# Performance work log

Measured on AMD Instinct MI355X. Metric: run time of the kernel, lower is better.

## Reference

```python
import jax, jax.numpy as jnp
import numpy as np

POOL_SIZE = 8
SEG_LEN = 100
N_CODEBOOKS = 4
VOCAB = 1024
EMB = 128
HID = 512
LAT = 256
NUM_CODES = 1024
BETA = 0.1
BATCH = 128


def _pool_matrix(T, P):
    # torch adaptive_avg_pool1d bin boundaries
    starts = np.floor(np.arange(P) * T / P).astype(int)
    ends = np.ceil((np.arange(P) + 1) * T / P).astype(int)
    M = np.zeros((T, P), np.float32)
    for i in range(P):
        M[starts[i]:ends[i], i] = 1.0 / (ends[i] - starts[i])
    return jnp.asarray(M)

_POOL = _pool_matrix(SEG_LEN, POOL_SIZE)


def _conv1d_same3(x, w, b):
    # x: (B, Cin, T), w: (Cout, Cin, 3), padding=1
    y = jax.lax.conv_general_dilated(x, w, (1,), [(1, 1)],
                                     dimension_numbers=('NCH', 'OIH', 'NCH'))
    return y + b[None, :, None]


def _encode(tokens, emb, c1w, c1b, c2w, c2b, c3w, c3b):
    # tokens: (B, T, C) int -> z_e (B, POOL_SIZE, LAT)
    B, T, C = tokens.shape
    x = emb[tokens]                      # (B, T, C, EMB)
    x = x.reshape(B, T, C * EMB).transpose(0, 2, 1)  # (B, C*EMB, T)
    x = jax.nn.relu(_conv1d_same3(x, c1w, c1b))
    x = jax.nn.relu(_conv1d_same3(x, c2w, c2b))
    x = jnp.einsum('bct,tp->bcp', x, _POOL)          # adaptive avg pool -> (B, HID, 8)
    x = jnp.einsum('bcp,oc->bpo', x, c3w[:, :, 0]) + c3b  # 1x1 conv -> (B, 8, LAT)
    return x


def _vq(z_e, codebook):
    # z_e: (B, L, D); eval-mode EMA quantizer (no buffer update)
    cb_sq = jnp.sum(codebook ** 2, axis=-1)          # (K,)
    dist = (jnp.sum(z_e ** 2, axis=-1, keepdims=True)
            - 2.0 * jnp.einsum('bld,kd->blk', z_e, codebook) + cb_sq)
    codes = jnp.argmin(dist, axis=-1)                # (B, L)
    z_q = codebook[codes]                            # gather (B, L, D)
    z_q_st = z_e + jax.lax.stop_gradient(z_q - z_e)
    commit = jnp.mean((z_e - jax.lax.stop_gradient(z_q)) ** 2)
    return z_q_st, codes, BETA * commit


def _decode(z_prev, z_curr, z_next, fc1w, fc1b, fc2w, fc2b, d1w, d1b, d2w, d2b):
    B = z_curr.shape[0]
    z = jnp.concatenate([z_prev, z_curr, z_next], axis=1).reshape(B, -1)  # (B, 3*8*LAT)
    h = jax.nn.relu(z @ fc1w.T + fc1b)
    h = jax.nn.relu(h @ fc2w.T + fc2b)               # (B, HID)
    h = jnp.broadcast_to(h[:, :, None], (B, HID, SEG_LEN))
    # ConvTranspose1d(k=3, pad=1, stride=1) == conv with flipped, transposed kernel
    w1 = jnp.flip(jnp.swapaxes(d1w, 0, 1), -1)       # (O, I, 3)
    h = jax.nn.relu(_conv1d_same3(h, w1, d1b))
    out = jnp.einsum('bct,cv->bvt', h, d2w[:, :, 0]) + d2b[None, :, None]  # (B, V*C, T)
    logits = out.reshape(B, N_CODEBOOKS, VOCAB, SEG_LEN).transpose(0, 3, 1, 2)
    return logits                                    # (B, T, C, V)


def _model(tokens_prev, tokens_curr, tokens_next, emb, conv1_w, conv1_b,
           conv2_w, conv2_b, conv3_w, conv3_b, codebook, fc1_w, fc1_b,
           fc2_w, fc2_b, deconv1_w, deconv1_b, deconv2_w, deconv2_b):
    enc = lambda t: _encode(t, emb, conv1_w, conv1_b, conv2_w, conv2_b, conv3_w, conv3_b)
    z_prev, _, vq_prev = _vq(enc(tokens_prev), codebook)
    z_curr, _, vq_curr = _vq(enc(tokens_curr), codebook)
    z_next, _, vq_next = _vq(enc(tokens_next), codebook)
    logits = _decode(z_prev, z_curr, z_next, fc1_w, fc1_b, fc2_w, fc2_b,
                     deconv1_w, deconv1_b, deconv2_w, deconv2_b)
    logp = jax.nn.log_softmax(logits, axis=-1)
    nll = -jnp.take_along_axis(logp, tokens_curr[..., None], axis=-1)[..., 0]
    recon_loss = jnp.mean(nll)
    vq_loss = vq_prev + vq_curr + vq_next
    centered = codebook - jnp.mean(codebook, axis=0, keepdims=True)
    diversity_loss = -jnp.mean(centered ** 2)
    total = recon_loss + vq_loss + 0.0 * diversity_loss  # variance_loss_scale=0.0
    return total


def setup_inputs() -> dict:
    key = jax.random.key(0)
    ks = jax.random.split(key, 20)
    s = 0.02
    n = lambda k, shape, sc=0.02: sc * jax.random.normal(k, shape, dtype=jnp.float32)
    return {
        'tokens_prev': jax.random.randint(ks[0], (BATCH, SEG_LEN, N_CODEBOOKS), 0, VOCAB),
        'tokens_curr': jax.random.randint(ks[1], (BATCH, SEG_LEN, N_CODEBOOKS), 0, VOCAB),
        'tokens_next': jax.random.randint(ks[2], (BATCH, SEG_LEN, N_CODEBOOKS), 0, VOCAB),
        'emb': n(ks[3], (VOCAB, EMB), 1.0),
        'conv1_w': n(ks[4], (HID, EMB * N_CODEBOOKS, 3)),
        'conv1_b': jnp.zeros((HID,), jnp.float32),
        'conv2_w': n(ks[5], (HID, HID, 3)),
        'conv2_b': jnp.zeros((HID,), jnp.float32),
        'conv3_w': n(ks[6], (LAT, HID, 1)),
        'conv3_b': jnp.zeros((LAT,), jnp.float32),
        'codebook': n(ks[7], (NUM_CODES, LAT), 1.0),
        'fc1_w': n(ks[8], (HID, LAT * POOL_SIZE * 3)),
        'fc1_b': jnp.zeros((HID,), jnp.float32),
        'fc2_w': n(ks[9], (HID, HID)),
        'fc2_b': jnp.zeros((HID,), jnp.float32),
        'deconv1_w': n(ks[10], (HID, HID, 3)),
        'deconv1_b': jnp.zeros((HID,), jnp.float32),
        'deconv2_w': n(ks[11], (HID, VOCAB * N_CODEBOOKS, 1)),
        'deconv2_b': jnp.zeros((VOCAB * N_CODEBOOKS,), jnp.float32),
    }


def reference(tokens_prev, tokens_curr, tokens_next, emb, conv1_w, conv1_b,
              conv2_w, conv2_b, conv3_w, conv3_b, codebook, fc1_w, fc1_b,
              fc2_w, fc2_b, deconv1_w, deconv1_b, deconv2_w, deconv2_b):
    return _model(tokens_prev, tokens_curr, tokens_next, emb, conv1_w, conv1_b,
                  conv2_w, conv2_b, conv3_w, conv3_b, codebook, fc1_w, fc1_b,
                  fc2_w, fc2_b, deconv1_w, deconv1_b, deconv2_w, deconv2_b)
```

## Files before the change

### kernel.cpp

```cpp
#include <hip/hip_runtime.h>
#include <math.h>

#define B_    128
#define T_    100
#define TPAD  104
#define CB_   4
#define EMB_  128
#define NROW  39936
#define ZOFF  131072

typedef __attribute__((ext_vector_type(8))) short short8;
typedef __attribute__((ext_vector_type(4))) short short4v;
typedef __attribute__((ext_vector_type(4))) float f32x4;

__device__ __forceinline__ short f2bf(float x) {
  unsigned u = __builtin_bit_cast(unsigned, x);
  u += 0x7fffu + ((u >> 16) & 1u);
  return (short)(u >> 16);
}
__device__ __forceinline__ float bf2f(short s) {
  unsigned u = ((unsigned)(unsigned short)s) << 16;
  return __builtin_bit_cast(float, u);
}

#define GLOAD_LDS(g, l) __builtin_amdgcn_global_load_lds( \
    (const __attribute__((address_space(1))) void*)(g),   \
    (__attribute__((address_space(3))) void*)(l), 16, 0, 0)

#define MFMA16(a, b, c) __builtin_amdgcn_mfma_f32_16x16x32_bf16(a, b, c, 0, 0, 0)
#define SWZ(row, slot) (((slot) + ((row) >> 1)) & 3)

#define STEP_SYNC() do {                                   \
    asm volatile("s_waitcnt vmcnt(0)" ::: "memory");       \
    __builtin_amdgcn_s_barrier();                          \
    __builtin_amdgcn_sched_barrier(0);                     \
  } while (0)

__global__ void k_prep(const float* __restrict__ emb,
                       const float* __restrict__ c1w, const float* __restrict__ c2w,
                       const float* __restrict__ c3w, const float* __restrict__ cbk,
                       const float* __restrict__ fc1w, const float* __restrict__ fc2w,
                       const float* __restrict__ d1w, const float* __restrict__ d2w,
                       short* __restrict__ YbS, short* __restrict__ embB,
                       short* __restrict__ Wb1, short* __restrict__ Wb2,
                       short* __restrict__ c3wB, short* __restrict__ cbkB,
                       short* __restrict__ fc1wB, short* __restrict__ fc2wB,
                       short* __restrict__ SB, short* __restrict__ d2wTB,
                       float* __restrict__ cbsq) {
  __shared__ float tile[32][33];
  int bid = blockIdx.x;
  int id = bid * 256 + threadIdx.x;
  if (bid < 24581) {
    if (id < 1024) {
      int row = id >> 9, c = id & 511;
      long off = row ? ((long)(NROW + 1) * 512 + c) : c;
      YbS[off] = 0;
    } else if (id < 132096) {
      int l = id - 1024;
      embB[l] = f2bf(emb[l]);
    } else if (id < 132224) {
      embB[ZOFF + (id - 132096)] = 0;
    } else if (id < 1705088) {
      int local = id - 132224;
      const float* w = (local < 786432) ? c1w : c2w;
      short* o = (local < 786432) ? Wb1 : Wb2;
      int l2 = (local < 786432) ? local : local - 786432;
      int i = l2 & 511, oo = (l2 >> 9) & 511, tap = l2 >> 18;
      o[l2] = f2bf(w[oo * 1536 + i * 3 + tap]);
    } else if (id < 1836160) {
      int l = id - 1705088;
      c3wB[l] = f2bf(c3w[l]);
    } else if (id < 2098304) {
      int l = id - 1836160;
      cbkB[l] = f2bf(cbk[l]);
    } else if (id < 5244032) {
      int l = id - 2098304;
      fc1wB[l] = f2bf(fc1w[l]);
    } else if (id < 5506176) {
      int l = id - 5244032;
      fc2wB[l] = f2bf(fc2w[l]);
    } else if (id < 6292608) {
      int l = id - 5506176;
      int i = l & 511, o = (l >> 9) & 511, cls = l >> 18;
      const float* w = d1w + (i * 512 + o) * 3;
      float v;
      if (cls == 0)      v = w[0] + w[1];
      else if (cls == 1) v = w[0] + w[1] + w[2];
      else               v = w[1] + w[2];
      SB[(cls * 512 + o) * 512 + i] = f2bf(v);
    }
  } else if (bid < 26629) {
    int blk = bid - 24581;
    int bx = blk & 127, by = blk >> 7;
    int tx = threadIdx.x & 31, ty = threadIdx.x >> 5;
    #pragma unroll
    for (int j = 0; j < 32; j += 8)
      tile[ty + j][tx] = d2w[(by * 32 + ty + j) * 4096 + bx * 32 + tx];
    __syncthreads();
    #pragma unroll
    for (int j = 0; j < 32; j += 8)
      d2wTB[(bx * 32 + ty + j) * 512 + by * 32 + tx] = f2bf(tile[tx][ty + j]);
  } else {
    int idx = (bid - 26629) * 256 + threadIdx.x;
    int row = idx >> 6, lane = threadIdx.x & 63;
    float4 v = *(const float4*)&cbk[row * 256 + lane * 4];
    float s = v.x * v.x + v.y * v.y + v.z * v.z + v.w * v.w;
    #pragma unroll
    for (int m = 1; m < 64; m <<= 1) s += __shfl_xor(s, m);
    if (lane == 0) cbsq[row] = s;
  }
}

__global__ __launch_bounds__(256) void k_conv1_embed(const int* __restrict__ tok0,
                                                     const int* __restrict__ tok1,
                                                     const int* __restrict__ tok2,
                                                     const short* __restrict__ embB,
                                                     const short* __restrict__ Wb,
                                                     const float* __restrict__ bias,
                                                     short* __restrict__ Y) {
  __shared__ short sm[2][16896];
  int r0 = blockIdx.y * 128;
  int o0 = blockIdx.x * 128;
  int tid = threadIdx.x;
  int lane = tid & 63, wid = tid >> 6;
  int wm = wid >> 1, wn = wid & 1;
  int ls = lane >> 4, lr = lane & 15;
  int g = ((lane & 3) - ((lane >> 3) & 3)) & 3;

  int toff[3][4];
  #pragma unroll
  for (int i = 0; i < 3; ++i) {
    int q = wid + 4 * i;
    if (q < 9) {
      int rr = r0 - 1 + 16 * q + (lane >> 2);
      bool ok = (rr >= 0) && (rr < NROW);
      int sb = ok ? (rr / 104) : 0;
      int t = rr - sb * 104;
      ok = ok && (t < T_);
      int b = sb & 127, s = sb >> 7;
      const int* tokp = (s == 0) ? tok0 : (s == 1) ? tok1 : tok2;
      if (ok) {
        int4 tv = *(const int4*)&tokp[(b * T_ + t) * CB_];
// ... 53 lines not shown
        int row = wm * 64 + m * 16 + lr + tap;
        a[m] = A8[row * 4 + SWZ(row, ls)];
      }
      #pragma unroll
      for (int n = 0; n < 4; ++n) {
        int row = wn * 64 + n * 16 + lr;
        b[n] = B8[(tap * 128 + row) * 4 + SWZ(row, ls)];
      }
      #pragma unroll
      for (int m = 0; m < 4; ++m)
        #pragma unroll
        for (int n = 0; n < 4; ++n)
          acc[m][n] = MFMA16(a[m], b[n], acc[m][n]);
    }
    STEP_SYNC();
  }
  #pragma unroll
  for (int m = 0; m < 4; ++m) {
    #pragma unroll
    for (int n = 0; n < 4; ++n) {
      int col = o0 + wn * 64 + n * 16 + lr;
      float bv = bias[col];
      #pragma unroll
      for (int j = 0; j < 4; ++j) {
        int r = r0 + wm * 64 + m * 16 + ls * 4 + j;
        int t = r % TPAD;
        float v = (t < T_) ? fmaxf(acc[m][n][j] + bv, 0.f) : 0.f;
        Y[(long)r * 512 + col] = f2bf(v);
      }
    }
  }
}

__global__ __launch_bounds__(256) void k_conv3_mfma(const short* __restrict__ X,
                                                    const short* __restrict__ Wb,
                                                    const float* __restrict__ bias,
                                                    short* __restrict__ Y) {
  __shared__ short sm[2][16896];
  int r0 = blockIdx.y * 128;
  int o0 = blockIdx.x * 128;
  int tid = threadIdx.x;
  int lane = tid & 63, wid = tid >> 6;
  int wm = wid >> 1, wn = wid & 1;
  int ls = lane >> 4, lr = lane & 15;
  int g = ((lane & 3) - ((lane >> 3) & 3)) & 3;
  long laneoff = (long)(lane >> 2) * 512 + g * 8;

  const short* gp[9];
  #pragma unroll
  for (int i = 0; i < 9; ++i) {
    int q = wid + 4 * i;
    if (q < 33) {
      long base;
      const short* src;
      if (q < 9) { src = X; base = (long)(r0 - 1 + 16 * q) * 512; }
      else {
        int b = q - 9, tap = b >> 3, j = b & 7;
        src = Wb; base = (long)(tap * 512 + o0 + 16 * j) * 512;
      }
      gp[i] = src + base + laneoff;
    }
  }

  #pragma unroll
  for (int i = 0; i < 9; ++i) {
    int q = wid + 4 * i;
    if (q < 33) { GLOAD_LDS(gp[i], &sm[0][q * 512]); gp[i] += 32; }
  }
  STEP_SYNC();

// ... 10 lines not shown
    }
    const short8* A8 = (const short8*)sm[cur];
    const short8* B8 = (const short8*)(sm[cur] + 4608);
    #pragma unroll
    for (int tap = 0; tap < 3; ++tap) {
      short8 a[4], b[4];
      #pragma unroll
      for (int m = 0; m < 4; ++m) {
        int row = wm * 64 + m * 16 + lr + tap;
        a[m] = A8[row * 4 + SWZ(row, ls)];
      }
      #pragma unroll
      for (int n = 0; n < 4; ++n) {
        int row = wn * 64 + n * 16 + lr;
        b[n] = B8[(tap * 128 + row) * 4 + SWZ(row, ls)];
      }
      #pragma unroll
      for (int m = 0; m < 4; ++m)
        #pragma unroll
        for (int n = 0; n < 4; ++n)
          acc[m][n] = MFMA16(a[m], b[n], acc[m][n]);
    }
    STEP_SYNC();
  }
  #pragma unroll
  for (int m = 0; m < 4; ++m) {
    #pragma unroll
    for (int n = 0; n < 4; ++n) {
      int col = o0 + wn * 64 + n * 16 + lr;
      float bv = bias[col];
      #pragma unroll
      for (int j = 0; j < 4; ++j) {
        int r = r0 + wm * 64 + m * 16 + ls * 4 + j;
        int t = r % TPAD;
        float v = (t < T_) ? fmaxf(acc[m][n][j] + bv, 0.f) : 0.f;
        Y[(long)r * 512 + col] = f2bf(v);
      }
    }
  }
}

__global__ __launch_bounds__(256) void k_gemm_mfma(const short* __restrict__ A,
                                                   const short* __restrict__ B,
                                                   float* __restrict__ C,
                                                   short* __restrict__ Cb,
                                                   const float* __restrict__ bias,
                                                   int K, int N, int relu) {
  __shared__ short sm[8192];
  int r0 = blockIdx.x * 128;
  int o0 = blockIdx.y * 128;
  int tid = threadIdx.x;
  int lane = tid & 63, wid = tid >> 6;
  int wm = wid >> 1, wn = wid & 1;
  int ls = lane >> 4, lr = lane & 15;
  int g = ((lane & 3) - ((lane >> 3) & 3)) & 3;
  long laneoff = (long)(lane >> 2) * K + g * 8;

  const short* gp[4];
  const short* lp[4];
  #pragma unroll
  for (int i = 0; i < 4; ++i) {
    int q = wid + 4 * i;
    const short* src;
    long base;
    if (q < 8) { src = A; base = (long)(r0 + 16 * q) * K; }
    else       { src = B; base = (long)(o0 + 16 * (q - 8)) * K; }
    gp[i] = src + base + laneoff;
    lp[i] = sm + q * 512;
  }

  f32x4 acc[4][4] = {};
  for (int kc = 0; kc < K; kc += 32) {
// ... 11 lines not shown
    for (int m = 0; m < 4; ++m) {
      int row = wm * 64 + m * 16 + lr;
      a[m] = A8[row * 4 + SWZ(row, ls)];
    }
    #pragma unroll
    for (int n = 0; n < 4; ++n) {
      int row = wn * 64 + n * 16 + lr;
      b[n] = B8[row * 4 + SWZ(row, ls)];
    }
    #pragma unroll
    for (int m = 0; m < 4; ++m)
      #pragma unroll
      for (int n = 0; n < 4; ++n)
        acc[m][n] = MFMA16(a[m], b[n], acc[m][n]);
  }
  #pragma unroll
  for (int m = 0; m < 4; ++m) {
    #pragma unroll
    for (int n = 0; n < 4; ++n) {
      int col = o0 + wn * 64 + n * 16 + lr;
      float bv = bias ? bias[col] : 0.f;
      #pragma unroll
      for (int j = 0; j < 4; ++j) {
        int r = r0 + wm * 64 + m * 16 + ls * 4 + j;
        float v = acc[m][n][j] + bv;
        if (relu) v = fmaxf(v, 0.f);
        C[(long)r * N + col] = v;
        if (Cb) Cb[(long)r * N + col] = f2bf(v);
      }
    }
  }
}

__global__ __launch_bounds__(256) void k_dot_argmin(const short* __restrict__ A,
                                                    const short* __restrict__ B,
                                                    const float* __restrict__ cbsq,
                                                    float* __restrict__ apv,
                                                    int* __restrict__ api) {
  __shared__ short sm[8192];
  __shared__ float svv[128][2];
  __shared__ int sii[128][2];
  const int K = 256;
  int r0 = blockIdx.x * 128;
  int o0 = blockIdx.y * 128;
  int tid = threadIdx.x;
  int lane = tid & 63, wid = tid >> 6;
  int wm = wid >> 1, wn = wid & 1;
  int ls = lane >> 4, lr = lane & 15;
  int g = ((lane & 3) - ((lane >> 3) & 3)) & 3;
  long laneoff = (long)(lane >> 2) * K + g * 8;

  const short* gp[4];
  const short* lp[4];
  #pragma unroll
  for (int i = 0; i < 4; ++i) {
    int q = wid + 4 * i;
    const short* src;
    long base;
    if (q < 8) { src = A; base = (long)(r0 + 16 * q) * K; }
    else       { src = B; base = (long)(o0 + 16 * (q - 8)) * K; }
    gp[i] = src + base + laneoff;
    lp[i] = sm + q * 512;
  }

  f32x4 acc[4][4] = {};
  #pragma unroll
  for (int kc = 0; kc < K; kc += 32) {
    __syncthreads();
    #pragma unroll
    for (int i = 0; i < 4; ++i) {
      GLOAD_LDS(gp[i], lp[i]);
      gp[i] += 32;
    }
    __syncthreads();
    const short8* A8 = (const short8*)sm;
    const short8* B8 = (const short8*)(sm + 4096);
    short8 a[4], b[4];
    #pragma unroll
    for (int m = 0; m < 4; ++m) {
      int row = wm * 64 + m * 16 + lr;
      a[m] = A8[row * 4 + SWZ(row, ls)];
    }
    #pragma unroll
    for (int n = 0; n < 4; ++n) {
      int row = wn * 64 + n * 16 + lr;
      b[n] = B8[row * 4 + SWZ(row, ls)];
    }
    #pragma unroll
    for (int m = 0; m < 4; ++m)
      #pragma unroll
      for (int n = 0; n < 4; ++n)
        acc[m][n] = MFMA16(a[m], b[n], acc[m][n]);
  }
  float cq[4];
  #pragma unroll
  for (int n = 0; n < 4; ++n) cq[n] = cbsq[o0 + wn * 64 + n * 16 + lr];
  #pragma unroll
  for (int m = 0; m < 4; ++m) {
    #pragma unroll
    for (int j = 0; j < 4; ++j) {
      float bv = 3.4e38f; int bi = 0x7fffffff;
      #pragma unroll
      for (int n = 0; n < 4; ++n) {
        int col = o0 + wn * 64 + n * 16 + lr;
        float v = cq[n] - 2.f * acc[m][n][j];
        if (v < bv || (v == bv && col < bi)) { bv = v; bi = col; }
      }
      #pragma unroll
      for (int d = 1; d < 16; d <<= 1) {
        float ov = __shfl_xor(bv, d);
        int oi = __shfl_xor(bi, d);
        if (ov < bv || (ov == bv && oi < bi)) { bv = ov; bi = oi; }
      }
      if (lr == 0) {
        int rl = wm * 64 + m * 16 + ls * 4 + j;
        svv[rl][wn] = bv;
        sii[rl][wn] = bi;
      }
    }
  }
  __syncthreads();
  if (tid < 128) {
    float v0 = svv[tid][0], v1 = svv[tid][1];
    int i0 = sii[tid][0], i1 = sii[tid][1];
    bool t1 = (v1 < v0) || (v1 == v0 && i1 < i0);
    apv[(long)(r0 + tid) * 8 + blockIdx.y] = t1 ? v1 : v0;
    api[(long)(r0 + tid) * 8 + blockIdx.y] = t1 ? i1 : i0;
  }
}

__global__ __launch_bounds__(256) void k_vq_combine(const float* __restrict__ apv,
                                                    const int* __restrict__ api,
                                                    const float* __restrict__ ze,
                                                    const float* __restrict__ cb,
                                                    const short* __restrict__ cbkB,
                                                    short* __restrict__ zallB,
                                                    float* __restrict__ commit_part) {
  __shared__ float sv[256];
  __shared__ int ksb;
  int row = blockIdx.x, tid = threadIdx.x;
  if (tid == 0) {
    float bv = apv[(long)row * 8]; int bi = api[(long)row * 8];
    #pragma unroll
    for (int j = 1; j < 8; ++j) {
      float v = apv[(long)row * 8 + j]; int i = api[(long)row * 8 + j];
      if (v < bv || (v == bv && i < bi)) { bv = v; bi = i; }
    }
    ksb = bi;
  }
  __syncthreads();
  int ks = ksb;
  float zq = cb[ks * 256 + tid];
  float zev = ze[(long)row * 256 + tid];
  int s = row >> 10, bp = row & 1023;
  int b = bp >> 3, p = bp & 7;
  zallB[b * 6144 + s * 2048 + p * 256 + tid] = cbkB[ks * 256 + tid];
  float d = zev - zq;
  sv[tid] = d * d;
  __syncthreads();
  for (int off = 128; off; off >>= 1) { if (tid < off) sv[tid] += sv[tid + off]; __syncthreads(); }
  if (tid == 0) commit_part[row] = sv[0];
}

__global__ __launch_bounds__(256) void k_gemm_mfma_sk(const short* __restrict__ A,
                                                      const short* __restrict__ B,
                                                      float* __restrict__ part,
                                                      int M, int N, int K,
                                                      int kchunk, int KS, long bgstride) {
  __shared__ short sm[8192];
  int r0 = blockIdx.x * 128;
  int o0 = blockIdx.y * 128;
  int bz = blockIdx.z;
  int g = bz / KS, zz = bz - g * KS;
  const short* Bg = B + (long)g * bgstride;
  int k0 = zz * kchunk;
  int tid = threadIdx.x;
  int lane = tid & 63, wid = tid >> 6;
  int wm = wid >> 1, wn = wid & 1;
  int ls = lane >> 4, lr = lane & 15;
  int gsl = ((lane & 3) - ((lane >> 3) & 3)) & 3;
  long laneoff = (long)(lane >> 2) * K + gsl * 8 + k0;

  const short* gp[4];
  const short* lp[4];
  #pragma unroll
  for (int i = 0; i < 4; ++i) {
    int q = wid + 4 * i;
    const short* src;
    long base;
    if (q < 8) { src = A;  base = (long)(r0 + 16 * q) * K; }
    else       { src = Bg; base = (long)(o0 + 16 * (q - 8)) * K; }
    gp[i] = src + base + laneoff;
    lp[i] = sm + q * 512;
  }
// ... 11 lines not shown
    const short8* B8 = (const short8*)(sm + 4096);
    short8 a[4], b[4];
    #pragma unroll
    for (int m = 0; m < 4; ++m) {
      int row = wm * 64 + m * 16 + lr;
      a[m] = A8[row * 4 + SWZ(row, ls)];
    }
    #pragma unroll
    for (int n = 0; n < 4; ++n) {
      int row = wn * 64 + n * 16 + lr;
      b[n] = B8[row * 4 + SWZ(row, ls)];
    }
    #pragma unroll
    for (int m = 0; m < 4; ++m)
      #pragma unroll
      for (int n = 0; n < 4; ++n)
        acc[m][n] = MFMA16(a[m], b[n], acc[m][n]);
  }
  float* P = part + (long)bz * M * N;
  #pragma unroll
  for (int m = 0; m < 4; ++m) {
    #pragma unroll
    for (int n = 0; n < 4; ++n) {
      int col = o0 + wn * 64 + n * 16 + lr;
      #pragma unroll
      for (int j = 0; j < 4; ++j) {
        int r = r0 + wm * 64 + m * 16 + ls * 4 + j;
        P[(long)r * N + col] = acc[m][n][j];
      }
    }
  }
}

__global__ void k_reduce_bf16(const float* __restrict__ part, short* __restrict__ Cb,
                              const float* __restrict__ bias, int N, int MN,
                              int KS, int relu, int total4) {
  int id = blockIdx.x * 256 + threadIdx.x;
  if (id >= total4) return;
  int e = id * 4;
  int g = e / MN;
  int rem = e - g * MN;
  const float* base = part + (long)g * KS * MN + rem;
  float4 s = *(const float4*)base;
  for (int j = 1; j < KS; ++j) {
    float4 v = *(const float4*)(base + (long)j * MN);
    s.x += v.x; s.y += v.y; s.z += v.z; s.w += v.w;
  }
  int c = rem % N;
  s.x += bias[c]; s.y += bias[c + 1]; s.z += bias[c + 2]; s.w += bias[c + 3];
  if (relu) {
    s.x = fmaxf(s.x, 0.f); s.y = fmaxf(s.y, 0.f);
    s.z = fmaxf(s.z, 0.f); s.w = fmaxf(s.w, 0.f);
  }
  short4v o;
  o[0] = f2bf(s.x); o[1] = f2bf(s.y); o[2] = f2bf(s.z); o[3] = f2bf(s.w);
  *(short4v*)&Cb[(long)g * MN + rem] = o;
}

__global__ void k_pool(const short* __restrict__ Xg, short* __restrict__ pooledB) {
  int id = blockIdx.x * 256 + threadIdx.x;
  int row = id >> 6, cg = id & 63;
  int s = row >> 10, bp = row & 1023;
  int b = bp >> 3, p = bp & 7;
  int t0 = (p * 25) >> 1;
  const short8* src = (const short8*)(Xg + (long)((s * 128 + b) * TPAD + t0) * 512) + cg;
  float acc[8] = {};
  #pragma unroll
  for (int j = 0; j < 13; ++j) {
    short8 v = src[j * 64];
    #pragma unroll
    for (int k = 0; k < 8; ++k) acc[k] += bf2f(v[k]);
  }
  short8 o;
  #pragma unroll
  for (int k = 0; k < 8; ++k) o[k] = f2bf(acc[k] * (1.f / 13.f));
  ((short8*)pooledB)[(long)row * 64 + cg] = o;
}

__global__ __launch_bounds__(256) void k_logits_lse_recon(const float* __restrict__ part,
                                                          const float* __restrict__ d2b,
                                                          const int* __restrict__ tok,
                                                          float* __restrict__ rpart2) {
  __shared__ float row[1024];
  __shared__ float sm[256];
  int blk = blockIdx.x;
  int cb_i = blk & 3, b = (blk >> 2) & 127, cls = blk >> 9;
  int m = cls * 128 + b;
  const float* p0 = part + (long)m * 4096 + cb_i * 1024;
  const float* p1 = p0 + (long)384 * 4096;
  const float* bb = d2b + cb_i * 1024;
  int tid = threadIdx.x;
  float v[4];
  #pragma unroll
  for (int j = 0; j < 4; ++j) {
    int c = tid + 256 * j;
    v[j] = p0[c] + p1[c] + bb[c];
    row[c] = v[j];
  }
  float mx = fmaxf(fmaxf(v[0], v[1]), fmaxf(v[2], v[3]));
  sm[tid] = mx; __syncthreads();
  for (int off = 128; off; off >>= 1) { if (tid < off) sm[tid] = fmaxf(sm[tid], sm[tid + off]); __syncthreads(); }
  float gm = sm[0]; __syncthreads();
  float e = expf(v[0] - gm) + expf(v[1] - gm) + expf(v[2] - gm) + expf(v[3] - gm);
  sm[tid] = e; __syncthreads();
  for (int off = 128; off; off >>= 1) { if (tid < off) sm[tid] += sm[tid + off]; __syncthreads(); }
  float lse = gm + logf(sm[0]);
  __syncthreads();
  float val = 0.f;
  if (cls == 1) {
    if (tid < 98) {
      int tk = tok[(b * T_ + tid + 1) * CB_ + cb_i];
      val = lse - row[tk];
    }
  } else if (tid == 0) {
    int t = (cls == 0) ? 0 : 99;
    int tk = tok[(b * T_ + t) * CB_ + cb_i];
    val = lse - row[tk];
  }
  sm[tid] = val; __syncthreads();
  for (int off = 128; off; off >>= 1) { if (tid < off) sm[tid] += sm[tid + off]; __syncthreads(); }
  if (tid == 0) rpart2[blk] = sm[0];
}

__global__ void k_final(const float* __restrict__ rpart2, const float* __restrict__ cpart,
                        float* __restrict__ out) {
  __shared__ float sm[256];
  __shared__ float rs;
  int tid = threadIdx.x;
  float r = 0.f;
  #pragma unroll
  for (int j = 0; j < 6; ++j) r += rpart2[tid + 256 * j];
  sm[tid] = r; __syncthreads();
  for (int off = 128; off; off >>= 1) { if (tid < off) sm[tid] += sm[tid + off]; __syncthreads(); }
  if (tid == 0) rs = sm[0];
  __syncthreads();
  float c = 0.f;
  #pragma unroll
  for (int j = 0; j < 12; ++j) c += cpart[tid + 256 * j];
  sm[tid] = c; __syncthreads();
  for (int off = 128; off; off >>= 1) { if (tid < off) sm[tid] += sm[tid + off]; __syncthreads(); }
  if (tid == 0) out[0] = rs / 51200.f + 0.1f * (sm[0] / 262144.f);
}

extern "C" void kernel_launch(void* const* d_in, const int* in_sizes, int n_in,
                              void* d_out, int out_size, void* d_ws, size_t ws_size,
                              hipStream_t stream) {
  const int*   tok_prev = (const int*)d_in[0];
  const int*   tok_curr = (const int*)d_in[1];
  const int*   tok_next = (const int*)d_in[2];
  const float* emb  = (const float*)d_in[3];
  const float* c1w  = (const float*)d_in[4];
  const float* c1b  = (const float*)d_in[5];
  const float* c2w  = (const float*)d_in[6];
  const float* c2b  = (const float*)d_in[7];
  const float* c3w  = (const float*)d_in[8];
  const float* c3b  = (const float*)d_in[9];
  const float* cbk  = (const float*)d_in[10];
  const float* fc1w = (const float*)d_in[11];
  const float* fc1b = (const float*)d_in[12];
  const float* fc2w = (const float*)d_in[13];
  const float* fc2b = (const float*)d_in[14];
  const float* d1w  = (const float*)d_in[15];
  const float* d1b  = (const float*)d_in[16];
  const float* d2w  = (const float*)d_in[17];
  const float* d2b  = (const float*)d_in[18];

  float* ws = (float*)d_ws;
  short* XbS = (short*)ws;
  short* YbS = (short*)(ws + 10224128);
  float* fp  = ws + 2 * 10224128;
  short* Wb1    = (short*)fp;
  short* Wb2    = (short*)(fp + 393216);
  short* c3wB   = (short*)(fp + 786432);
  short* cbkB   = (short*)(fp + 851968);
  short* pooledB= (short*)(fp + 983040);
  float* ze     = fp + 1769472;
  short* zeB    = (short*)(fp + 2555904);
  short* fc1wB  = (short*)(fp + 2949120);
  short* fc2wB  = (short*)(fp + 4521984);
  short* SB     = (short*)(fp + 4653056);
  short* d2wTB  = (short*)(fp + 5046272);
  float* part   = fp + 6094848;
  float* cbsq   = part + 3145728;
  short* zallB  = (short*)(cbsq + 1024);
  float* cpart  = cbsq + 1024 + 393216;
  short* h1B    = (short*)(cpart + 3072);
  short* h2B    = (short*)(cpart + 35840);
  short* h2cB   = (short*)(cpart + 68608);
  float* rpart2 = cpart + 166912;
  float* apv    = cpart + 168448;
  int*   api    = (int*)(cpart + 193024);
  short* embB   = (short*)(cpart + 217600);

  const short* Yv = YbS + 512;
  short* Xc = XbS + 512;

  k_prep<<<26885, 256, 0, stream>>>(emb, c1w, c2w, c3w, cbk, fc1w, fc2w, d1w, d2w,
                                    YbS, embB, Wb1, Wb2, c3wB, cbkB, fc1wB, fc2wB,
                                    SB, d2wTB, cbsq);

  k_conv1_embed<<<dim3(4, 312), 256, 0, stream>>>(tok_prev, tok_curr, tok_next,
                                                  embB, Wb1, c1b, (short*)Yv);
  k_conv3_mfma <<<dim3(4, 312), 256, 0, stream>>>(Yv, Wb2, c2b, Xc);
  k_pool       <<<768, 256, 0, stream>>>(Xc, pooledB);
  k_gemm_mfma  <<<dim3(24, 2), 256, 0, stream>>>(pooledB, c3wB, ze, zeB, c3b, 512, 256, 0);
  k_dot_argmin <<<dim3(24, 8), 256, 0, stream>>>(zeB, cbkB, cbsq, apv, api);
  k_vq_combine <<<3072, 256, 0, stream>>>(apv, api, ze, cbk, cbkB, zallB, cpart);

  k_gemm_mfma_sk<<<dim3(1, 4, 16), 256, 0, stream>>>(zallB, fc1wB, part, 128, 512, 6144, 384, 16, 0);
  k_reduce_bf16 <<<64, 256, 0, stream>>>(part, h1B, fc1b, 512, 65536, 16, 1, 16384);
  k_gemm_mfma_sk<<<dim3(1, 4, 8), 256, 0, stream>>>(h1B, fc2wB, part, 128, 512, 512, 64, 8, 0);
  k_reduce_bf16 <<<64, 256, 0, stream>>>(part, h2B, fc2b, 512, 65536, 8, 1, 16384);
  k_gemm_mfma_sk<<<dim3(1, 4, 24), 256, 0, stream>>>(h2B, SB, part, 128, 512, 512, 64, 8, 262144);
  k_reduce_bf16 <<<192, 256, 0, stream>>>(part, h2cB, d1b, 512, 65536, 8, 1, 49152);
  k_gemm_mfma_sk<<<dim3(3, 32, 2), 256, 0, stream>>>(h2cB, d2wTB, part, 384, 4096, 512, 256, 2, 0);
  k_logits_lse_recon<<<1536, 256, 0, stream>>>(part, d2b, tok_curr, rpart2);

  k_final<<<1, 256, 0, stream>>>(rpart2, cpart, (float*)d_out);
}
```

Measured before the change: 260.3 us.

## Fold conv3 into codebook distances and fuse split-K reductions into next GEMM

```diff
diff --git a/kernel.cpp b/kernel.cpp
--- a/kernel.cpp
+++ b/kernel.cpp
@@ -38,19 +38,21 @@
 
 __global__ void k_prep(const float* __restrict__ emb,
                        const float* __restrict__ c1w, const float* __restrict__ c2w,
-                       const float* __restrict__ c3w, const float* __restrict__ cbk,
+                       const float* __restrict__ c3w, const float* __restrict__ c3b,
+                       const float* __restrict__ cbk,
                        const float* __restrict__ fc1w, const float* __restrict__ fc2w,
                        const float* __restrict__ d1w, const float* __restrict__ d2w,
                        short* __restrict__ YbS, short* __restrict__ embB,
                        short* __restrict__ Wb1, short* __restrict__ Wb2,
-                       short* __restrict__ c3wB, short* __restrict__ cbkB,
+                       short* __restrict__ c3wB, short* __restrict__ c3wT,
+                       short* __restrict__ cbkB,
                        short* __restrict__ fc1wB, short* __restrict__ fc2wB,
                        short* __restrict__ SB, short* __restrict__ d2wTB,
-                       float* __restrict__ cbsq) {
+                       float* __restrict__ cbsq2) {
   __shared__ float tile[32][33];
   int bid = blockIdx.x;
   int id = bid * 256 + threadIdx.x;
-  if (bid < 24581) {
+  if (bid < 25093) {
     if (id < 1024) {
       int row = id >> 9, c = id & 511;
       long off = row ? ((long)(NROW + 1) * 512 + c) : c;
@@ -70,17 +72,21 @@
     } else if (id < 1836160) {
       int l = id - 1705088;
       c3wB[l] = f2bf(c3w[l]);
-    } else if (id < 2098304) {
+    } else if (id < 1967232) {
       int l = id - 1836160;
+      int o = l & 255, i = l >> 8;
+      c3wT[l] = f2bf(c3w[o * 512 + i]);
+    } else if (id < 2229376) {
+      int l = id - 1967232;
       cbkB[l] = f2bf(cbk[l]);
-    } else if (id < 5244032) {
-      int l = id - 2098304;
+    } else if (id < 5375104) {
+      int l = id - 2229376;
       fc1wB[l] = f2bf(fc1w[l]);
-    } else if (id < 5506176) {
-      int l = id - 5244032;
+    } else if (id < 5637248) {
+      int l = id - 5375104;
       fc2wB[l] = f2bf(fc2w[l]);
-    } else if (id < 6292608) {
-      int l = id - 5506176;
+    } else if (id < 6423680) {
+      int l = id - 5637248;
       int i = l & 511, o = (l >> 9) & 511, cls = l >> 18;
       const float* w = d1w + (i * 512 + o) * 3;
       float v;
@@ -89,8 +95,8 @@
       else               v = w[1] + w[2];
       SB[(cls * 512 + o) * 512 + i] = f2bf(v);
     }
-  } else if (bid < 26629) {
-    int blk = bid - 24581;
+  } else if (bid < 27141) {
+    int blk = bid - 25093;
     int bx = blk & 127, by = blk >> 7;
     int tx = threadIdx.x & 31, ty = threadIdx.x >> 5;
     #pragma unroll
@@ -101,13 +107,15 @@
     for (int j = 0; j < 32; j += 8)
       d2wTB[(bx * 32 + ty + j) * 512 + by * 32 + tx] = f2bf(tile[tx][ty + j]);
   } else {
-    int idx = (bid - 26629) * 256 + threadIdx.x;
+    int idx = (bid - 27141) * 256 + threadIdx.x;
     int row = idx >> 6, lane = threadIdx.x & 63;
     float4 v = *(const float4*)&cbk[row * 256 + lane * 4];
+    float4 bb = *(const float4*)&c3b[lane * 4];
     float s = v.x * v.x + v.y * v.y + v.z * v.z + v.w * v.w;
-    #pragma unroll
-    for (int m = 1; m < 64; m <<= 1) s += __shfl_xor(s, m);
-    if (lane == 0) cbsq[row] = s;
+    float s2 = v.x * bb.x + v.y * bb.y + v.z * bb.z + v.w * bb.w;
+    #pragma unroll
+    for (int m = 1; m < 64; m <<= 1) { s += __shfl_xor(s, m); s2 += __shfl_xor(s2, m); }
+    if (lane == 0) cbsq2[row] = s - 2.f * s2;
   }
 }
 
@@ -390,15 +398,12 @@
   }
 }
 
-__global__ __launch_bounds__(256) void k_dot_argmin(const short* __restrict__ A,
-                                                    const short* __restrict__ B,
-                                                    const float* __restrict__ cbsq,
-                                                    float* __restrict__ apv,
-                                                    int* __restrict__ api) {
+__global__ __launch_bounds__(256) void k_zesq(const short* __restrict__ A,
+                                              const short* __restrict__ B,
+                                              const float* __restrict__ bias,
+                                              float* __restrict__ zs) {
   __shared__ short sm[8192];
-  __shared__ float svv[128][2];
-  __shared__ int sii[128][2];
-  const int K = 256;
+  const int K = 512;
   int r0 = blockIdx.x * 128;
   int o0 = blockIdx.y * 128;
   int tid = threadIdx.x;
@@ -422,7 +427,6 @@
   }
 
   f32x4 acc[4][4] = {};
-  #pragma unroll
   for (int kc = 0; kc < K; kc += 32) {
     __syncthreads();
     #pragma unroll
@@ -450,9 +454,88 @@
       for (int n = 0; n < 4; ++n)
         acc[m][n] = MFMA16(a[m], b[n], acc[m][n]);
   }
+  float s = 0.f;
+  #pragma unroll
+  for (int n = 0; n < 4; ++n) {
+    float bv = bias[o0 + wn * 64 + n * 16 + lr];
+    #pragma unroll
+    for (int m = 0; m < 4; ++m)
+      #pragma unroll
+      for (int j = 0; j < 4; ++j) {
+        float v = acc[m][n][j] + bv;
+        s += v * v;
+      }
+  }
+  __syncthreads();
+  float* red = (float*)sm;
+  red[tid] = s;
+  __syncthreads();
+  for (int off = 128; off; off >>= 1) { if (tid < off) red[tid] += red[tid + off]; __syncthreads(); }
+  if (tid == 0) zs[blockIdx.y * 24 + blockIdx.x] = red[0];
+}
+
+__global__ __launch_bounds__(256) void k_dot_argmin(const short* __restrict__ A,
+                                                    const short* __restrict__ B,
+                                                    const float* __restrict__ cbsq2,
+                                                    float* __restrict__ apv,
+                                                    int* __restrict__ api) {
+  __shared__ short sm[8192];
+  __shared__ float svv[128][2];
+  __shared__ int sii[128][2];
+  const int K = 512;
+  int r0 = blockIdx.x * 128;
+  int o0 = blockIdx.y * 128;
+  int tid = threadIdx.x;
+  int lane = tid & 63, wid = tid >> 6;
+  int wm = wid >> 1, wn = wid & 1;
+  int ls = lane >> 4, lr = lane & 15;
+  int g = ((lane & 3) - ((lane >> 3) & 3)) & 3;
+  long laneoff = (long)(lane >> 2) * K + g * 8;
+
+  const short* gp[4];
+  const short* lp[4];
+  #pragma unroll
+  for (int i = 0; i < 4; ++i) {
+    int q = wid + 4 * i;
+    const short* src;
+    long base;
+    if (q < 8) { src = A; base = (long)(r0 + 16 * q) * K; }
+    else       { src = B; base = (long)(o0 + 16 * (q - 8)) * K; }
+    gp[i] = src + base + laneoff;
+    lp[i] = sm + q * 512;
+  }
+
+  f32x4 acc[4][4] = {};
+  for (int kc = 0; kc < K; kc += 32) {
+    __syncthreads();
+    #pragma unroll
+    for (int i = 0; i < 4; ++i) {
+      GLOAD_LDS(gp[i], lp[i]);
+      gp[i] += 32;
+    }
+    __syncthreads();
+    const short8* A8 = (const short8*)sm;
+    const short8* B8 = (const short8*)(sm + 4096);
+    short8 a[4], b[4];
+    #pragma unroll
+    for (int m = 0; m < 4; ++m) {
+      int row = wm * 64 + m * 16 + lr;
+      a[m] = A8[row * 4 + SWZ(row, ls)];
+    }
+    #pragma unroll
+    for (int n = 0; n < 4; ++n) {
+      int row = wn * 64 + n * 16 + lr;
+      b[n] = B8[row * 4 + SWZ(row, ls)];
+    }
+    #pragma unroll
+    for (int m = 0; m < 4; ++m)
+      #pragma unroll
+      for (int n = 0; n < 4; ++n)
+        acc[m][n] = MFMA16(a[m], b[n], acc[m][n]);
+  }
   float cq[4];
   #pragma unroll
-  for (int n = 0; n < 4; ++n) cq[n] = cbsq[o0 + wn * 64 + n * 16 + lr];
+  for (int n = 0; n < 4; ++n) cq[n] = cbsq2[o0 + wn * 64 + n * 16 + lr];
   #pragma unroll
   for (int m = 0; m < 4; ++m) {
     #pragma unroll
@@ -489,35 +572,35 @@
 
 __global__ __launch_bounds__(256) void k_vq_combine(const float* __restrict__ apv,
                                                     const int* __restrict__ api,
-                                                    const float* __restrict__ ze,
-                                                    const float* __restrict__ cb,
                                                     const short* __restrict__ cbkB,
                                                     short* __restrict__ zallB,
-                                                    float* __restrict__ commit_part) {
-  __shared__ float sv[256];
-  __shared__ int ksb;
-  int row = blockIdx.x, tid = threadIdx.x;
-  if (tid == 0) {
-    float bv = apv[(long)row * 8]; int bi = api[(long)row * 8];
-    #pragma unroll
-    for (int j = 1; j < 8; ++j) {
-      float v = apv[(long)row * 8 + j]; int i = api[(long)row * 8 + j];
-      if (v < bv || (v == bv && i < bi)) { bv = v; bi = i; }
-    }
-    ksb = bi;
-  }
-  __syncthreads();
-  int ks = ksb;
-  float zq = cb[ks * 256 + tid];
-  float zev = ze[(long)row * 256 + tid];
+                                                    float* __restrict__ cpart) {
+  __shared__ float cm[8];
+  int tid = threadIdx.x;
+  int rg = tid >> 5, lt = tid & 31;
+  int lane = tid & 63;
+  int row = blockIdx.x * 8 + rg;
+  float v = 3.4e38f; int idx = 0x7fffffff;
+  if (lt < 8) { v = apv[(long)row * 8 + lt]; idx = api[(long)row * 8 + lt]; }
+  #pragma unroll
+  for (int d = 1; d < 8; d <<= 1) {
+    float ov = __shfl_xor(v, d);
+    int oi = __shfl_xor(idx, d);
+    if (ov < v || (ov == v && oi < idx)) { v = ov; idx = oi; }
+  }
+  int ks = __shfl(idx, lane & 32);
   int s = row >> 10, bp = row & 1023;
   int b = bp >> 3, p = bp & 7;
-  zallB[b * 6144 + s * 2048 + p * 256 + tid] = cbkB[ks * 256 + tid];
-  float d = zev - zq;
-  sv[tid] = d * d;
+  ((short8*)zallB)[(b * 6144 + s * 2048 + p * 256) / 8 + lt] =
+      ((const short8*)cbkB)[ks * 32 + lt];
+  if (lt == 0) cm[rg] = v;
   __syncthreads();
-  for (int off = 128; off; off >>= 1) { if (tid < off) sv[tid] += sv[tid + off]; __syncthreads(); }
-  if (tid == 0) commit_part[row] = sv[0];
+  if (tid == 0) {
+    float c = 0.f;
+    #pragma unroll
+    for (int j = 0; j < 8; ++j) c += cm[j];
+    cpart[blockIdx.x] = c;
+  }
 }
 
 __global__ __launch_bounds__(256) void k_gemm_mfma_sk(const short* __restrict__ A,
@@ -595,6 +678,96 @@
   }
 }
 
+__global__ __launch_bounds__(256) void k_gemm_sk_ared(const float* __restrict__ Apart,
+                                                      int KSa,
+                                                      const float* __restrict__ abias,
+                                                      const short* __restrict__ B,
+                                                      float* __restrict__ part,
+                                                      int KS, long bgstride) {
+  __shared__ short smem[16384];
+  int o0 = blockIdx.y * 128;
+  int bz = blockIdx.z;
+  int g = bz / KS, zz = bz - g * KS;
+  const short* Bg = B + (long)g * bgstride;
+  int k0 = zz * 64;
+  int tid = threadIdx.x;
+  int lane = tid & 63, wid = tid >> 6;
+  int wm = wid >> 1, wn = wid & 1;
+  int ls = lane >> 4, lr = lane & 15;
+  int gsw = ((lane & 3) - ((lane >> 3) & 3)) & 3;
+
+  #pragma unroll
+  for (int i = 0; i < 4; ++i) {
+    int idx = wid + 4 * i;
+    int step = idx >> 3, j = idx & 7;
+    const short* gp = Bg + (long)(o0 + 16 * j) * 512 + k0 + step * 32
+                    + (long)(lane >> 2) * 512 + gsw * 8;
+    GLOAD_LDS(gp, smem + 8192 + idx * 512);
+  }
+  #pragma unroll
+  for (int t = 0; t < 4; ++t) {
+    int slot = tid + 256 * t;
+    int step = slot >> 9, rem = slot & 511;
+    int row = rem >> 2, sl = rem & 3;
+    int gp2 = (sl - ((row >> 1) & 3)) & 3;
+    int col = k0 + step * 32 + gp2 * 8;
+    const float* ap = Apart + (long)row * 512 + col;
+    float s0 = 0, s1 = 0, s2 = 0, s3 = 0, s4 = 0, s5 = 0, s6 = 0, s7 = 0;
+    for (int j = 0; j < KSa; ++j) {
+      const float* p = ap + (long)j * 65536;
+      float4 a0 = *(const float4*)p;
+      float4 a1 = *(const float4*)(p + 4);
+      s0 += a0.x; s1 += a0.y; s2 += a0.z; s3 += a0.w;
+      s4 += a1.x; s5 += a1.y; s6 += a1.z; s7 += a1.w;
+    }
+    float4 b0 = *(const float4*)&abias[col];
+    float4 b1 = *(const float4*)&abias[col + 4];
+    short8 o;
+    o[0] = f2bf(fmaxf(s0 + b0.x, 0.f)); o[1] = f2bf(fmaxf(s1 + b0.y, 0.f));
+    o[2] = f2bf(fmaxf(s2 + b0.z, 0.f)); o[3] = f2bf(fmaxf(s3 + b0.w, 0.f));
+    o[4] = f2bf(fmaxf(s4 + b1.x, 0.f)); o[5] = f2bf(fmaxf(s5 + b1.y, 0.f));
+    o[6] = f2bf(fmaxf(s6 + b1.z, 0.f)); o[7] = f2bf(fmaxf(s7 + b1.w, 0.f));
+    ((short8*)smem)[step * 512 + row * 4 + sl] = o;
+  }
+  __syncthreads();
+
+  f32x4 acc[4][4] = {};
+  #pragma unroll
+  for (int step = 0; step < 2; ++step) {
+    const short8* A8 = (const short8*)smem + step * 512;
+    const short8* B8 = (const short8*)(smem + 8192) + step * 512;
+    short8 a[4], b[4];
+    #pragma unroll
+    for (int m = 0; m < 4; ++m) {
+      int row = wm * 64 + m * 16 + lr;
+      a[m] = A8[row * 4 + SWZ(row, ls)];
+    }
+    #pragma unroll
+    for (int n = 0; n < 4; ++n) {
+      int row = wn * 64 + n * 16 + lr;
+      b[n] = B8[row * 4 + SWZ(row, ls)];
+    }
+    #pragma unroll
+    for (int m = 0; m < 4; ++m)
+      #pragma unroll
+      for (int n = 0; n < 4; ++n)
+        acc[m][n] = MFMA16(a[m], b[n], acc[m][n]);
+  }
+  float* P = part + (long)bz * 65536;
+  #pragma unroll
+  for (int m = 0; m < 4; ++m) {
+    #pragma unroll
+    for (int n = 0; n < 4; ++n) {
+      int col = o0 + wn * 64 + n * 16 + lr;
+      #pragma unroll
+      for (int j = 0; j < 4; ++j) {
+        int r = wm * 64 + m * 16 + ls * 4 + j;
+        P[(long)r * 512 + col] = acc[m][n][j];
+      }
+    }
+  }
+}
+
 __global__ void k_reduce_bf16(const float* __restrict__ part, short* __restrict__ Cb,
                               const float* __restrict__ bias, int N, int MN,
                               int KS, int relu, int total4) {
@@ -650,14 +823,13 @@
   int cb_i = blk & 3, b = (blk >> 2) & 127, cls = blk >> 9;
   int m = cls * 128 + b;
   const float* p0 = part + (long)m * 4096 + cb_i * 1024;
-  const float* p1 = p0 + (long)384 * 4096;
   const float* bb = d2b + cb_i * 1024;
   int tid = threadIdx.x;
   float v[4];
   #pragma unroll
   for (int j = 0; j < 4; ++j) {
     int c = tid + 256 * j;
-    v[j] = p0[c] + p1[c] + bb[c];
+    v[j] = p0[c] + bb[c];
     row[c] = v[j];
   }
   float mx = fmaxf(fmaxf(v[0], v[1]), fmaxf(v[2], v[3]));
@@ -686,7 +858,7 @@
 }
 
 __global__ void k_final(const float* __restrict__ rpart2, const float* __restrict__ cpart,
-                        float* __restrict__ out) {
+                        const float* __restrict__ zesq, float* __restrict__ out) {
   __shared__ float sm[256];
   __shared__ float rs;
   int tid = threadIdx.x;
@@ -697,9 +869,9 @@
   for (int off = 128; off; off >>= 1) { if (tid < off) sm[tid] += sm[tid + off]; __syncthreads(); }
   if (tid == 0) rs = sm[0];
   __syncthreads();
-  float c = 0.f;
-  #pragma unroll
-  for (int j = 0; j < 12; ++j) c += cpart[tid + 256 * j];
+  float c = cpart[tid];
+  if (tid < 128) c += cpart[tid + 256];
+  if (tid < 48)  c += zesq[tid];
   sm[tid] = c; __syncthreads();
   for (int off = 128; off; off >>= 1) { if (tid < off) sm[tid] += sm[tid + off]; __syncthreads(); }
   if (tid == 0) out[0] = rs / 51200.f + 0.1f * (sm[0] / 262144.f);
@@ -735,49 +907,50 @@
   short* Wb1    = (short*)fp;
   short* Wb2    = (short*)(fp + 393216);
   short* c3wB   = (short*)(fp + 786432);
-  short* cbkB   = (short*)(fp + 851968);
-  short* pooledB= (short*)(fp + 983040);
-  float* ze     = fp + 1769472;
-  short* zeB    = (short*)(fp + 2555904);
-  short* fc1wB  = (short*)(fp + 2949120);
-  short* fc2wB  = (short*)(fp + 4521984);
-  short* SB     = (short*)(fp + 4653056);
-  short* d2wTB  = (short*)(fp + 5046272);
-  float* part   = fp + 6094848;
-  float* cbsq   = part + 3145728;
-  short* zallB  = (short*)(cbsq + 1024);
-  float* cpart  = cbsq + 1024 + 393216;
-  short* h1B    = (short*)(cpart + 3072);
-  short* h2B    = (short*)(cpart + 35840);
-  short* h2cB   = (short*)(cpart + 68608);
-  float* rpart2 = cpart + 166912;
-  float* apv    = cpart + 168448;
-  int*   api    = (int*)(cpart + 193024);
-  short* embB   = (short*)(cpart + 217600);
+  short* c3wT   = (short*)(fp + 851968);
+  short* cbkB   = (short*)(fp + 917504);
+  short* MwB    = (short*)(fp + 1048576);
+  short* pooledB= (short*)(fp + 1310720);
+  short* fc1wB  = (short*)(fp + 2097152);
+  short* fc2wB  = (short*)(fp + 3670016);
+  short* SB     = (short*)(fp + 3801088);
+  short* d2wTB  = (short*)(fp + 4194304);
+  float* partA  = fp + 5242880;
+  float* partB  = fp + 6291456;
+  float* partC  = fp + 6815744;
+  float* partD  = fp + 8388608;
+  float* cbsq2  = fp + 9961472;
+  short* zallB  = (short*)(fp + 9962496);
+  float* cpart  = fp + 10355712;
+  float* zesq   = fp + 10356096;
+  short* h2cB   = (short*)(fp + 10356160);
+  float* rpart2 = fp + 10454464;
+  float* apv    = fp + 10456000;
+  int*   api    = (int*)(fp + 10480576);
+  short* embB   = (short*)(fp + 10505152);
 
   const short* Yv = YbS + 512;
   short* Xc = XbS + 512;
 
-  k_prep<<<26885, 256, 0, stream>>>(emb, c1w, c2w, c3w, cbk, fc1w, fc2w, d1w, d2w,
-                                    YbS, embB, Wb1, Wb2, c3wB, cbkB, fc1wB, fc2wB,
-                                    SB, d2wTB, cbsq);
+  k_prep<<<27397, 256, 0, stream>>>(emb, c1w, c2w, c3w, c3b, cbk, fc1w, fc2w, d1w, d2w,
+                                    YbS, embB, Wb1, Wb2, c3wB, c3wT, cbkB, fc1wB, fc2wB,
+                                    SB, d2wTB, cbsq2);
+  k_gemm_mfma<<<dim3(8, 4), 256, 0, stream>>>(cbkB, c3wT, partA, MwB, nullptr, 256, 512, 0);
 
   k_conv1_embed<<<dim3(4, 312), 256, 0, stream>>>(tok_prev, tok_curr, tok_next,
                                                   embB, Wb1, c1b, (short*)Yv);
   k_conv3_mfma <<<dim3(4, 312), 256, 0, stream>>>(Yv, Wb2, c2b, Xc);
   k_pool       <<<768, 256, 0, stream>>>(Xc, pooledB);
-  k_gemm_mfma  <<<dim3(24, 2), 256, 0, stream>>>(pooledB, c3wB, ze, zeB, c3b, 512, 256, 0);
-  k_dot_argmin <<<dim3(24, 8), 256, 0, stream>>>(zeB, cbkB, cbsq, apv, api);
-  k_vq_combine <<<3072, 256, 0, stream>>>(apv, api, ze, cbk, cbkB, zallB, cpart);
-
-  k_gemm_mfma_sk<<<dim3(1, 4, 16), 256, 0, stream>>>(zallB, fc1wB, part, 128, 512, 6144, 384, 16, 0);
-  k_reduce_bf16 <<<64, 256, 0, stream>>>(part, h1B, fc1b, 512, 65536, 16, 1, 16384);
-  k_gemm_mfma_sk<<<dim3(1, 4, 8), 256, 0, stream>>>(h1B, fc2wB, part, 128, 512, 512, 64, 8, 0);
-  k_reduce_bf16 <<<64, 256, 0, stream>>>(part, h2B, fc2b, 512, 65536, 8, 1, 16384);
-  k_gemm_mfma_sk<<<dim3(1, 4, 24), 256, 0, stream>>>(h2B, SB, part, 128, 512, 512, 64, 8, 262144);
-  k_reduce_bf16 <<<192, 256, 0, stream>>>(part, h2cB, d1b, 512, 65536, 8, 1, 49152);
-  k_gemm_mfma_sk<<<dim3(3, 32, 2), 256, 0, stream>>>(h2cB, d2wTB, part, 384, 4096, 512, 256, 2, 0);
-  k_logits_lse_recon<<<1536, 256, 0, stream>>>(part, d2b, tok_curr, rpart2);
-
-  k_final<<<1, 256, 0, stream>>>(rpart2, cpart, (float*)d_out);
-}
+  k_zesq       <<<dim3(24, 2), 256, 0, stream>>>(pooledB, c3wB, c3b, zesq);
+  k_dot_argmin <<<dim3(24, 8), 256, 0, stream>>>(pooledB, MwB, cbsq2, apv, api);
+  k_vq_combine <<<384, 256, 0, stream>>>(apv, api, cbkB, zallB, cpart);
+
+  k_gemm_mfma_sk<<<dim3(1, 4, 16), 256, 0, stream>>>(zallB, fc1wB, partA, 128, 512, 6144, 384, 16, 0);
+  k_gemm_sk_ared<<<dim3(1, 4, 8),  256, 0, stream>>>(partA, 16, fc1b, fc2wB, partB, 8, 0);
+  k_gemm_sk_ared<<<dim3(1, 4, 24), 256, 0, stream>>>(partB, 8, fc2b, SB, partC, 8, 262144);
+  k_reduce_bf16 <<<192, 256, 0, stream>>>(partC, h2cB, d1b, 512, 65536, 8, 1, 49152);
+  k_gemm_mfma_sk<<<dim3(3, 32, 1), 256, 0, stream>>>(h2cB, d2wTB, partD, 384, 4096, 512, 512, 1, 0);
+  k_logits_lse_recon<<<1536, 256, 0, stream>>>(partD, d2b, tok_curr, rpart2);
+
+  k_final<<<1, 256, 0, stream>>>(rpart2, cpart, zesq, (float*)d_out);
+}
```

Measured after the change: 290.3 us, median of 3. 1.12x slower.

## Fuse adaptive average pooling into conv2 epilogue via atomics; drop final split-K

Applied to the files above, without the earlier changes.

```diff
diff --git a/kernel.cpp b/kernel.cpp
--- a/kernel.cpp
+++ b/kernel.cpp
@@ -46,11 +46,11 @@
                        short* __restrict__ c3wB, short* __restrict__ cbkB,
                        short* __restrict__ fc1wB, short* __restrict__ fc2wB,
                        short* __restrict__ SB, short* __restrict__ d2wTB,
-                       float* __restrict__ cbsq) {
+                       float* __restrict__ cbsq, float* __restrict__ pooled) {
   __shared__ float tile[32][33];
   int bid = blockIdx.x;
   int id = bid * 256 + threadIdx.x;
-  if (bid < 24581) {
+  if (bid < 30724) {
     if (id < 1024) {
       int row = id >> 9, c = id & 511;
       long off = row ? ((long)(NROW + 1) * 512 + c) : c;
@@ -88,9 +88,11 @@
       else if (cls == 1) v = w[0] + w[1] + w[2];
       else               v = w[1] + w[2];
       SB[(cls * 512 + o) * 512 + i] = f2bf(v);
-    }
-  } else if (bid < 26629) {
-    int blk = bid - 24581;
+    } else {
+      pooled[id - 6292608] = 0.f;
+    }
+  } else if (bid < 32772) {
+    int blk = bid - 30724;
     int bx = blk & 127, by = blk >> 7;
     int tx = threadIdx.x & 31, ty = threadIdx.x >> 5;
     #pragma unroll
@@ -101,7 +103,7 @@
     for (int j = 0; j < 32; j += 8)
       d2wTB[(bx * 32 + ty + j) * 512 + by * 32 + tx] = f2bf(tile[tx][ty + j]);
   } else {
-    int idx = (bid - 26629) * 256 + threadIdx.x;
+    int idx = (bid - 32772) * 256 + threadIdx.x;
     int row = idx >> 6, lane = threadIdx.x & 63;
     float4 v = *(const float4*)&cbk[row * 256 + lane * 4];
     float s = v.x * v.x + v.y * v.y + v.z * v.z + v.w * v.w;
@@ -227,10 +229,10 @@
   }
 }
 
-__global__ __launch_bounds__(256) void k_conv3_mfma(const short* __restrict__ X,
+__global__ __launch_bounds__(256) void k_conv2_pool(const short* __restrict__ X,
                                                     const short* __restrict__ Wb,
                                                     const float* __restrict__ bias,
-                                                    short* __restrict__ Y) {
+                                                    float* __restrict__ pooled) {
   __shared__ short sm[2][16896];
   int r0 = blockIdx.y * 128;
   int o0 = blockIdx.x * 128;
@@ -307,12 +309,29 @@
       #pragma unroll
       for (int j = 0; j < 4; ++j) {
         int r = r0 + wm * 64 + m * 16 + ls * 4 + j;
-        int t = r % TPAD;
-        float v = (t < T_) ? fmaxf(acc[m][n][j] + bv, 0.f) : 0.f;
-        Y[(long)r * 512 + col] = f2bf(v);
-      }
-    }
-  }
+        int sb = r / 104;
+        int t = r - sb * 104;
+        if (t < T_) {
+          float v = fmaxf(acc[m][n][j] + bv, 0.f) * (1.f / 13.f);
+          int plo = (2 * t) / 25;
+          int phi = (2 * t + 1) / 25;
+          atomicAdd(&pooled[(long)(sb * 8 + plo) * 512 + col], v);
+          if (phi != plo)
+            atomicAdd(&pooled[(long)(sb * 8 + phi) * 512 + col], v);
+        }
+      }
+    }
+  }
+}
+
+__global__ void k_poolcvt(const float* __restrict__ pooled, short* __restrict__ pooledB) {
+  int id = blockIdx.x * 256 + threadIdx.x;
+  float4 a0 = *(const float4*)&pooled[(long)id * 8];
+  float4 a1 = *(const float4*)&pooled[(long)id * 8 + 4];
+  short8 o;
+  o[0] = f2bf(a0.x); o[1] = f2bf(a0.y); o[2] = f2bf(a0.z); o[3] = f2bf(a0.w);
+  o[4] = f2bf(a1.x); o[5] = f2bf(a1.y); o[6] = f2bf(a1.z); o[7] = f2bf(a1.w);
+  ((short8*)pooledB)[id] = o;
 }
 
 __global__ __launch_bounds__(256) void k_gemm_mfma(const short* __restrict__ A,
@@ -620,26 +639,6 @@
   *(short4v*)&Cb[(long)g * MN + rem] = o;
 }
 
-__global__ void k_pool(const short* __restrict__ Xg, short* __restrict__ pooledB) {
-  int id = blockIdx.x * 256 + threadIdx.x;
-  int row = id >> 6, cg = id & 63;
-  int s = row >> 10, bp = row & 1023;
-  int b = bp >> 3, p = bp & 7;
-  int t0 = (p * 25) >> 1;
-  const short8* src = (const short8*)(Xg + (long)((s * 128 + b) * TPAD + t0) * 512) + cg;
-  float acc[8] = {};
-  #pragma unroll
-  for (int j = 0; j < 13; ++j) {
-    short8 v = src[j * 64];
-    #pragma unroll
-    for (int k = 0; k < 8; ++k) acc[k] += bf2f(v[k]);
-  }
-  short8 o;
-  #pragma unroll
-  for (int k = 0; k < 8; ++k) o[k] = f2bf(acc[k] * (1.f / 13.f));
-  ((short8*)pooledB)[(long)row * 64 + cg] = o;
-}
-
 __global__ __launch_bounds__(256) void k_logits_lse_recon(const float* __restrict__ part,
                                                           const float* __restrict__ d2b,
                                                           const int* __restrict__ tok,
@@ -650,14 +649,13 @@
   int cb_i = blk & 3, b = (blk >> 2) & 127, cls = blk >> 9;
   int m = cls * 128 + b;
   const float* p0 = part + (long)m * 4096 + cb_i * 1024;
-  const float* p1 = p0 + (long)384 * 4096;
   const float* bb = d2b + cb_i * 1024;
   int tid = threadIdx.x;
   float v[4];
   #pragma unroll
   for (int j = 0; j < 4; ++j) {
     int c = tid + 256 * j;
-    v[j] = p0[c] + p1[c] + bb[c];
+    v[j] = p0[c] + bb[c];
     row[c] = v[j];
   }
   float mx = fmaxf(fmaxf(v[0], v[1]), fmaxf(v[2], v[3]));
@@ -729,43 +727,42 @@
   const float* d2b  = (const float*)d_in[18];
 
   float* ws = (float*)d_ws;
-  short* XbS = (short*)ws;
-  short* YbS = (short*)(ws + 10224128);
-  float* fp  = ws + 2 * 10224128;
+  short* YbS = (short*)ws;
+  float* fp  = ws + 10224128;
   short* Wb1    = (short*)fp;
   short* Wb2    = (short*)(fp + 393216);
   short* c3wB   = (short*)(fp + 786432);
   short* cbkB   = (short*)(fp + 851968);
-  short* pooledB= (short*)(fp + 983040);
-  float* ze     = fp + 1769472;
-  short* zeB    = (short*)(fp + 2555904);
-  short* fc1wB  = (short*)(fp + 2949120);
-  short* fc2wB  = (short*)(fp + 4521984);
-  short* SB     = (short*)(fp + 4653056);
-  short* d2wTB  = (short*)(fp + 5046272);
-  float* part   = fp + 6094848;
-  float* cbsq   = part + 3145728;
-  short* zallB  = (short*)(cbsq + 1024);
-  float* cpart  = cbsq + 1024 + 393216;
-  short* h1B    = (short*)(cpart + 3072);
-  short* h2B    = (short*)(cpart + 35840);
-  short* h2cB   = (short*)(cpart + 68608);
-  float* rpart2 = cpart + 166912;
-  float* apv    = cpart + 168448;
-  int*   api    = (int*)(cpart + 193024);
-  short* embB   = (short*)(cpart + 217600);
+  float* pooled = fp + 983040;
+  short* pooledB= (short*)(fp + 2555904);
+  float* ze     = fp + 3342336;
+  short* zeB    = (short*)(fp + 4128768);
+  short* fc1wB  = (short*)(fp + 4521984);
+  short* fc2wB  = (short*)(fp + 6094848);
+  short* SB     = (short*)(fp + 6225920);
+  short* d2wTB  = (short*)(fp + 6619136);
+  float* part   = fp + 7667712;
+  float* cbsq   = fp + 10813440;
+  short* zallB  = (short*)(fp + 10814464);
+  float* cpart  = fp + 11207680;
+  short* h1B    = (short*)(fp + 11210752);
+  short* h2B    = (short*)(fp + 11243520);
+  short* h2cB   = (short*)(fp + 11276288);
+  float* rpart2 = fp + 11374592;
+  float* apv    = fp + 11376128;
+  int*   api    = (int*)(fp + 11400704);
+  short* embB   = (short*)(fp + 11425280);
 
   const short* Yv = YbS + 512;
-  short* Xc = XbS + 512;
-
-  k_prep<<<26885, 256, 0, stream>>>(emb, c1w, c2w, c3w, cbk, fc1w, fc2w, d1w, d2w,
+
+  k_prep<<<33028, 256, 0, stream>>>(emb, c1w, c2w, c3w, cbk, fc1w, fc2w, d1w, d2w,
                                     YbS, embB, Wb1, Wb2, c3wB, cbkB, fc1wB, fc2wB,
-                                    SB, d2wTB, cbsq);
+                                    SB, d2wTB, cbsq, pooled);
 
   k_conv1_embed<<<dim3(4, 312), 256, 0, stream>>>(tok_prev, tok_curr, tok_next,
                                                   embB, Wb1, c1b, (short*)Yv);
-  k_conv3_mfma <<<dim3(4, 312), 256, 0, stream>>>(Yv, Wb2, c2b, Xc);
-  k_pool       <<<768, 256, 0, stream>>>(Xc, pooledB);
+  k_conv2_pool <<<dim3(4, 312), 256, 0, stream>>>(Yv, Wb2, c2b, pooled);
+  k_poolcvt    <<<768, 256, 0, stream>>>(pooled, pooledB);
   k_gemm_mfma  <<<dim3(24, 2), 256, 0, stream>>>(pooledB, c3wB, ze, zeB, c3b, 512, 256, 0);
   k_dot_argmin <<<dim3(24, 8), 256, 0, stream>>>(zeB, cbkB, cbsq, apv, api);
   k_vq_combine <<<3072, 256, 0, stream>>>(apv, api, ze, cbk, cbkB, zallB, cpart);
@@ -776,7 +773,7 @@
   k_reduce_bf16 <<<64, 256, 0, stream>>>(part, h2B, fc2b, 512, 65536, 8, 1, 16384);
   k_gemm_mfma_sk<<<dim3(1, 4, 24), 256, 0, stream>>>(h2B, SB, part, 128, 512, 512, 64, 8, 262144);
   k_reduce_bf16 <<<192, 256, 0, stream>>>(part, h2cB, d1b, 512, 65536, 8, 1, 49152);
-  k_gemm_mfma_sk<<<dim3(3, 32, 2), 256, 0, stream>>>(h2cB, d2wTB, part, 384, 4096, 512, 256, 2, 0);
+  k_gemm_mfma_sk<<<dim3(3, 32, 1), 256, 0, stream>>>(h2cB, d2wTB, part, 384, 4096, 512, 512, 1, 0);
   k_logits_lse_recon<<<1536, 256, 0, stream>>>(part, d2b, tok_curr, rpart2);
 
   k_final<<<1, 256, 0, stream>>>(rpart2, cpart, (float*)d_out);
```

Result: slower. 414.5 us (+59.2%).
